# Performance work log

Hardware: AMD Instinct MI355X
Metric: run time of the kernel (lower is better)

The kernel has to match this reference:

```python
import jax, jax.numpy as jnp
import numpy as np
import math

IN_CH = 1024
OUT_CH = 512
T_DIM = 512
CLIP = 8
HEADS = 8
BS = 8192


def setup_inputs() -> dict:
    key = jax.random.key(0)
    ks = jax.random.split(key, 12)
    s = 0.02
    return {
        "x": jax.random.normal(ks[0], (BS * CLIP, IN_CH), dtype=jnp.float32),
        "t": jax.random.normal(ks[1], (BS, 1, T_DIM), dtype=jnp.float32),
        "W_down": jax.random.normal(ks[2], (OUT_CH, IN_CH), dtype=jnp.float32) * s,
        "b_down": jax.random.normal(ks[3], (OUT_CH,), dtype=jnp.float32) * s,
        "W_t": jax.random.normal(ks[4], (OUT_CH, T_DIM), dtype=jnp.float32) * s,
        "b_t": jax.random.normal(ks[5], (OUT_CH,), dtype=jnp.float32) * s,
        "W_qkv": jax.random.normal(ks[6], (3 * OUT_CH, OUT_CH), dtype=jnp.float32) * s,
        "b_qkv": jax.random.normal(ks[7], (3 * OUT_CH,), dtype=jnp.float32) * s,
        "W_out": jax.random.normal(ks[8], (OUT_CH, OUT_CH), dtype=jnp.float32) * s,
        "b_out": jax.random.normal(ks[9], (OUT_CH,), dtype=jnp.float32) * s,
    }


def reference(x, t, W_down, b_down, W_t, b_t, W_qkv, b_qkv, W_out, b_out):
    # down projection (in_channel != out_channels branch)
    x = x @ W_down.T + b_down                       # [bs*clip, out_ch]
    x = x.reshape(-1, CLIP, OUT_CH)                 # [bs, clip, out_ch]
    # time embedding (broadcast over clip dim)
    x = x + (t @ W_t.T + b_t)                       # [bs, clip, out_ch]
    qkv = x @ W_qkv.T + b_qkv                       # [bs, clip, 3*out_ch]
    bs, length, width = qkv.shape
    ch = width // (3 * HEADS)                       # 64
    q, k, v = jnp.split(qkv, 3, axis=2)             # each [bs, clip, out_ch]
    scale = 1.0 / math.sqrt(math.sqrt(ch))
    # NOTE: faithful to torch .view semantics (head-interleaved reshape)
    qh = (q * scale).reshape(bs * HEADS, length, ch)
    kh = (k * scale).reshape(bs * HEADS, length, ch)
    vh = v.reshape(bs * HEADS, length, ch)
    w = jnp.einsum('bqc,bkc->bqk', qh, kh)          # [bs*heads, clip, clip]
    w = jax.nn.softmax(w.astype(jnp.float32), axis=-1).astype(qkv.dtype)
    attn = jnp.einsum('bqk,bkc->bqc', w, vh).reshape(bs, length, -1)
    return attn @ W_out.T + b_out                   # [bs, clip, out_ch]
```

## Files before the change

### kernel.cpp

```cpp
#include <hip/hip_runtime.h>
#include <hip/hip_bf16.h>
#include <cstdint>
#include <cstddef>

typedef __bf16 bf16_t;
typedef __bf16 bf16x8 __attribute__((ext_vector_type(8)));
typedef float  f32x4  __attribute__((ext_vector_type(4)));

#define N_ROWS 65536
#define IN_CH  1024
#define OUT_CH 512
#define T_DIM  512
#define BS_    8192

__device__ __forceinline__ void async_copy16(const bf16_t* g, bf16_t* l) {
    __builtin_amdgcn_global_load_lds(
        (const __attribute__((address_space(1))) void*)(uintptr_t)(g),
        (__attribute__((address_space(3))) void*)(uintptr_t)(l),
        16, 0, 0);
}

__global__ __launch_bounds__(256)
void cvt_f32_bf16(const float* __restrict__ in, bf16_t* __restrict__ out, long n8) {
    long idx = (long)blockIdx.x * 256 + threadIdx.x;
    if (idx >= n8) return;
    const float4* p = (const float4*)(in + idx * 8);
    float4 u = p[0], v = p[1];
    bf16x8 o;
    o[0] = (__bf16)u.x; o[1] = (__bf16)u.y; o[2] = (__bf16)u.z; o[3] = (__bf16)u.w;
    o[4] = (__bf16)v.x; o[5] = (__bf16)v.y; o[6] = (__bf16)v.z; o[7] = (__bf16)v.w;
    *(bf16x8*)(out + idx * 8) = o;
}

__global__ __launch_bounds__(256)
void cvt_multi(const float* __restrict__ s0, bf16_t* __restrict__ d0, long n0,
               const float* __restrict__ s1, bf16_t* __restrict__ d1, long n1,
               const float* __restrict__ s2, bf16_t* __restrict__ d2, long n2,
               const float* __restrict__ s3, bf16_t* __restrict__ d3, long n3)
{
    long idx = (long)blockIdx.x * 256 + threadIdx.x;
    const float* s; bf16_t* d;
    if (idx < n0)                { s = s0; d = d0; }
    else if ((idx -= n0) < n1)   { s = s1; d = d1; }
    else if ((idx -= n1) < n2)   { s = s2; d = d2; }
    else if ((idx -= n2) < n3)   { s = s3; d = d3; }
    else return;
    const float4* p = (const float4*)(s + idx * 8);
    float4 u = p[0], v = p[1];
    bf16x8 o;
    o[0] = (__bf16)u.x; o[1] = (__bf16)u.y; o[2] = (__bf16)u.z; o[3] = (__bf16)u.w;
    o[4] = (__bf16)v.x; o[5] = (__bf16)v.y; o[6] = (__bf16)v.z; o[7] = (__bf16)v.w;
    *(bf16x8*)(d + idx * 8) = o;
}

__global__ __launch_bounds__(256)
void transpose_cvt(const float* __restrict__ in, bf16_t* __restrict__ out) {
    __shared__ float tile[64][65];
    const int bx = blockIdx.x;
    const int by = blockIdx.y;
    const int tx = threadIdx.x & 63;
    const int ty = threadIdx.x >> 6;
    #pragma unroll
    for (int r = 0; r < 64; r += 4)
        tile[r + ty][tx] = in[(size_t)(by * 64 + r + ty) * 1024 + bx * 64 + tx];
    __syncthreads();
    #pragma unroll
    for (int r = 0; r < 64; r += 4)
        out[(size_t)(bx * 64 + r + ty) * 512 + by * 64 + tx] = (bf16_t)tile[tx][r + ty];
}

template<int BIAS_MODE, typename CT>
__global__ __launch_bounds__(256, 3)
void gemm_bt(const bf16_t* __restrict__ A, const bf16_t* __restrict__ B,
             CT* __restrict__ C,
             const float* __restrict__ bias,
             const float* __restrict__ bias2,
             int M, int N, int K)
{
    __shared__ bf16_t sA[128 * 32];
    __shared__ bf16_t sB[128 * 32];

    const int tid  = threadIdx.x;
    const int wave = tid >> 6;
    const int lane = tid & 63;

    const int row0 = blockIdx.y * 128;
    const int col0 = blockIdx.x * 128;

    const int wr = (wave >> 1) * 64;
    const int wc = (wave & 1) * 64;

    f32x4 acc[4][4];
    #pragma unroll
    for (int i = 0; i < 4; ++i)
        #pragma unroll
        for (int j = 0; j < 4; ++j)
            acc[i][j] = (f32x4){0.f, 0.f, 0.f, 0.f};

    const int seg0  = wave * 2;
    const int srow  = lane >> 2;
    const int schnk = (lane & 3) * 8;

    const bf16_t* Abase = A + (size_t)row0 * K + (size_t)srow * K + schnk;
    const bf16_t* Bbase = B + (size_t)col0 * K + (size_t)srow * K + schnk;

    const int fr = lane & 15;
    const int fk = (lane >> 4) * 8;

    for (int k0 = 0; k0 < K; k0 += 32) {
        #pragma unroll
        for (int j2 = 0; j2 < 2; ++j2) {
            const int seg = seg0 + j2;
            async_copy16(Abase + (size_t)(seg * 16) * K + k0, sA + seg * 512);
            async_copy16(Bbase + (size_t)(seg * 16) * K + k0, sB + seg * 512);
        }
        __syncthreads();

        bf16x8 af[4], bfr[4];
        #pragma unroll
        for (int i = 0; i < 4; ++i)
            af[i] = *(const bf16x8*)(sA + (wr + i * 16 + fr) * 32 + fk);
        #pragma unroll
        for (int j = 0; j < 4; ++j)
            bfr[j] = *(const bf16x8*)(sB + (wc + j * 16 + fr) * 32 + fk);

        #pragma unroll
        for (int i = 0; i < 4; ++i)
            #pragma unroll
            for (int j = 0; j < 4; ++j)
                acc[i][j] = __builtin_amdgcn_mfma_f32_16x16x32_bf16(af[i], bfr[j], acc[i][j], 0, 0, 0);
        __syncthreads();
    }

    #pragma unroll
    for (int j = 0; j < 4; ++j) {
        const int gc = col0 + wc + j * 16 + (lane & 15);
        float cb = 0.f;
        if constexpr (BIAS_MODE == 0) cb = bias[gc];
        if constexpr (BIAS_MODE == 2) cb = bias[gc] + bias2[gc];
        #pragma unroll
        for (int i = 0; i < 4; ++i) {
            const int gr0 = row0 + wr + i * 16 + ((lane >> 4) << 2);
            #pragma unroll
            for (int r = 0; r < 4; ++r) {
                const int gr = gr0 + r;
                float v = acc[i][j][r];
                if constexpr (BIAS_MODE == 1)
                    v += bias2[(size_t)(gr >> 3) * N + gc];
                else
                    v += cb;
                C[(size_t)gr * N + gc] = (CT)v;
            }
        }
    }
}

__global__ __launch_bounds__(256, 4)
void attn_kernel(const bf16_t* __restrict__ qkv, bf16_t* __restrict__ out)
{
    __shared__ bf16_t skv[4][1024];
    const int tid  = threadIdx.x;
    const int wave = tid >> 6;
    const int lane = tid & 63;
    const size_t row = (size_t)blockIdx.x * 4 + wave;

    const bf16_t* base = qkv + row * 1536;
    bf16x8 q8 = *(const bf16x8*)(base + lane * 8);
    bf16x8 k8 = *(const bf16x8*)(base + 512 + lane * 8);
    bf16x8 v8 = *(const bf16x8*)(base + 1024 + lane * 8);
    *(bf16x8*)&skv[wave][lane * 8]       = k8;
    *(bf16x8*)&skv[wave][512 + lane * 8] = v8;

    float q[8];
    #pragma unroll
    for (int e = 0; e < 8; ++e) q[e] = (float)q8[e];
    __syncthreads();

    const int s8 = (lane & 7) * 8;
    float S[8];
    #pragma unroll
    for (int j = 0; j < 8; ++j) {
        bf16x8 kj = *(const bf16x8*)&skv[wave][j * 64 + s8];
        float p = 0.f;
        #pragma unroll
        for (int e = 0; e < 8; ++e) p += q[e] * (float)kj[e];
        p += __shfl_xor(p, 1);
        p += __shfl_xor(p, 2);
        p += __shfl_xor(p, 4);
        S[j] = p * 0.125f;
    }
    float m = S[0];
    #pragma unroll
    for (int j = 1; j < 8; ++j) m = fmaxf(m, S[j]);
    float sum = 0.f;
    #pragma unroll
    for (int j = 0; j < 8; ++j) { S[j] = __expf(S[j] - m); sum += S[j]; }
    const float inv = 1.f / sum;

    float o[8] = {0.f, 0.f, 0.f, 0.f, 0.f, 0.f, 0.f, 0.f};
    #pragma unroll
    for (int j = 0; j < 8; ++j) {
        const float pj = S[j] * inv;
        bf16x8 vj = *(const bf16x8*)&skv[wave][512 + j * 64 + s8];
        #pragma unroll
        for (int e = 0; e < 8; ++e) o[e] += pj * (float)vj[e];
    }
    bf16x8 o8;
    #pragma unroll
    for (int e = 0; e < 8; ++e) o8[e] = (__bf16)o[e];
    *(bf16x8*)(out + row * 512 + lane * 8) = o8;
}

extern "C" void kernel_launch(void* const* d_in, const int* in_sizes, int n_in,
                              void* d_out, int out_size, void* d_ws, size_t ws_size,
                              hipStream_t stream)
{
    const float* x      = (const float*)d_in[0];
    const float* t      = (const float*)d_in[1];
    const float* W_down = (const float*)d_in[2];
    const float* b_down = (const float*)d_in[3];
    const float* W_t    = (const float*)d_in[4];
    const float* b_t    = (const float*)d_in[5];
    const float* W_qkv  = (const float*)d_in[6];
    const float* b_qkv  = (const float*)d_in[7];
    const float* W_out  = (const float*)d_in[8];
    const float* b_out  = (const float*)d_in[9];
    float* out = (float*)d_out;

    char* p = (char*)d_ws;
    bf16_t* xb     = (bf16_t*)(p);
    bf16_t* qkvm   = (bf16_t*)(p + 134217728);
    bf16_t* am     = (bf16_t*)(p + 335544320);
    float*  tbias2 = (float*) (p + 402653184);
    bf16_t* tin    = (bf16_t*)(p + 452984832);
    bf16_t* tb     = (bf16_t*)(p + 461373440);
    bf16_t* wdT    = (bf16_t*)(p + 469762048);
    bf16_t* wt     = (bf16_t*)(p + 470810624);
    bf16_t* wq     = (bf16_t*)(p + 471334912);
    bf16_t* wo     = (bf16_t*)(p + 472907776);
    bf16_t* wf     = (bf16_t*)(p + 473432064);

    cvt_f32_bf16<<<32768, 256, 0, stream>>>(x, xb, (long)N_ROWS * IN_CH / 8);
    cvt_multi<<<2688, 256, 0, stream>>>(
        t,     tin, (long)BS_ * T_DIM / 8,
        W_qkv, wq,  (long)3 * OUT_CH * OUT_CH / 8,
        W_t,   wt,  (long)OUT_CH * T_DIM / 8,
        W_out, wo,  (long)OUT_CH * OUT_CH / 8);
    transpose_cvt<<<dim3(16, 8), 256, 0, stream>>>(W_down, wdT);

    gemm_bt<3, bf16_t><<<dim3(8, 12), 256, 0, stream>>>(
        wq, wdT, wf, nullptr, nullptr, 3 * OUT_CH, IN_CH, OUT_CH);

    gemm_bt<2, bf16_t><<<dim3(4, 64), 256, 0, stream>>>(
        tin, wt, tb, b_t, b_down, BS_, OUT_CH, T_DIM);

    gemm_bt<0, float><<<dim3(12, 64), 256, 0, stream>>>(
        tb, wq, tbias2, b_qkv, nullptr, BS_, 3 * OUT_CH, OUT_CH);

    gemm_bt<1, bf16_t><<<dim3(12, 512), 256, 0, stream>>>(
        xb, wf, qkvm, nullptr, tbias2, N_ROWS, 3 * OUT_CH, IN_CH);

    attn_kernel<<<16384, 256, 0, stream>>>(qkvm, am);

    gemm_bt<0, float><<<dim3(4, 512), 256, 0, stream>>>(
        am, wo, out, b_out, nullptr, N_ROWS, OUT_CH, OUT_CH);
}
```

Before: 873.4 us.

## Fuse attention with output projection and swizzle GEMM LDS tiles

Attention now writes its per-row outputs into shared memory, and the same block then runs the output-projection GEMM on those 32 rows with the full 512-wide W_out. This removes the round trip of the intermediate attention tensor through global memory and one kernel launch. The generic GEMM also gets an XOR swizzle on its LDS tiles to cut bank conflicts, and the broadcast time-bias in mode 1 is staged once in shared memory instead of being read from global memory per element. In exchange, the fused kernel uses more LDS, runs at lower occupancy, and does the attention part serially per wave with no overlap with the MFMA phase.

Result: slower. 894.4 us (+2.4%).

```diff
diff --git a/kernel.cpp b/kernel.cpp
--- a/kernel.cpp
+++ b/kernel.cpp
@@ -77,8 +77,9 @@
              const float* __restrict__ bias2,
              int M, int N, int K)
 {
-    __shared__ bf16_t sA[128 * 32];
-    __shared__ bf16_t sB[128 * 32];
+    __shared__ __align__(16) bf16_t sA[128 * 32];
+    __shared__ __align__(16) bf16_t sB[128 * 32];
+    __shared__ float stb[(BIAS_MODE == 1) ? 16 * 132 : 4];
 
     const int tid  = threadIdx.x;
     const int wave = tid >> 6;
@@ -90,6 +91,14 @@
     const int wr = (wave >> 1) * 64;
     const int wc = (wave & 1) * 64;
 
+    if constexpr (BIAS_MODE == 1) {
+        const int br = tid >> 4;
+        const int bc = (tid & 15) * 8;
+        const float* bsrc = bias2 + ((size_t)(row0 >> 3) + br) * N + col0 + bc;
+        *(float4*)&stb[br * 132 + bc]     = *(const float4*)(bsrc);
+        *(float4*)&stb[br * 132 + bc + 4] = *(const float4*)(bsrc + 4);
+    }
+
     f32x4 acc[4][4];
     #pragma unroll
     for (int i = 0; i < 4; ++i)
@@ -99,13 +108,14 @@
 
     const int seg0  = wave * 2;
     const int srow  = lane >> 2;
-    const int schnk = (lane & 3) * 8;
+    const int schnk = (((lane & 3) ^ (srow & 3)) * 8);
 
     const bf16_t* Abase = A + (size_t)row0 * K + (size_t)srow * K + schnk;
     const bf16_t* Bbase = B + (size_t)col0 * K + (size_t)srow * K + schnk;
 
     const int fr = lane & 15;
-    const int fk = (lane >> 4) * 8;
+    const int hi = lane >> 4;
+    const int swz = (hi ^ (fr & 3)) * 8;
 
     for (int k0 = 0; k0 < K; k0 += 32) {
         #pragma unroll
@@ -119,10 +129,10 @@
         bf16x8 af[4], bfr[4];
         #pragma unroll
         for (int i = 0; i < 4; ++i)
-            af[i] = *(const bf16x8*)(sA + (wr + i * 16 + fr) * 32 + fk);
+            af[i] = *(const bf16x8*)(sA + (wr + i * 16 + fr) * 32 + swz);
         #pragma unroll
         for (int j = 0; j < 4; ++j)
-            bfr[j] = *(const bf16x8*)(sB + (wc + j * 16 + fr) * 32 + fk);
+            bfr[j] = *(const bf16x8*)(sB + (wc + j * 16 + fr) * 32 + swz);
 
         #pragma unroll
         for (int i = 0; i < 4; ++i)
@@ -134,81 +144,141 @@
 
     #pragma unroll
     for (int j = 0; j < 4; ++j) {
-        const int gc = col0 + wc + j * 16 + (lane & 15);
+        const int gc = col0 + wc + j * 16 + fr;
         float cb = 0.f;
         if constexpr (BIAS_MODE == 0) cb = bias[gc];
         if constexpr (BIAS_MODE == 2) cb = bias[gc] + bias2[gc];
         #pragma unroll
         for (int i = 0; i < 4; ++i) {
-            const int gr0 = row0 + wr + i * 16 + ((lane >> 4) << 2);
+            const int lr0 = wr + i * 16 + hi * 4;
             #pragma unroll
             for (int r = 0; r < 4; ++r) {
-                const int gr = gr0 + r;
                 float v = acc[i][j][r];
                 if constexpr (BIAS_MODE == 1)
-                    v += bias2[(size_t)(gr >> 3) * N + gc];
+                    v += stb[((lr0 + r) >> 3) * 132 + wc + j * 16 + fr];
                 else
                     v += cb;
-                C[(size_t)gr * N + gc] = (CT)v;
+                C[(size_t)(row0 + lr0 + r) * N + gc] = (CT)v;
             }
         }
     }
 }
 
-__global__ __launch_bounds__(256, 4)
-void attn_kernel(const bf16_t* __restrict__ qkv, bf16_t* __restrict__ out)
+__global__ __launch_bounds__(256, 2)
+void attn_out(const bf16_t* __restrict__ qkv, const bf16_t* __restrict__ Wo,
+              const float* __restrict__ bias, float* __restrict__ C)
 {
-    __shared__ bf16_t skv[4][1024];
+    __shared__ __align__(16) bf16_t sa[32 * 512];
+    __shared__ __align__(16) bf16_t sB[512 * 32];
+
     const int tid  = threadIdx.x;
     const int wave = tid >> 6;
     const int lane = tid & 63;
-    const size_t row = (size_t)blockIdx.x * 4 + wave;
-
-    const bf16_t* base = qkv + row * 1536;
-    bf16x8 q8 = *(const bf16x8*)(base + lane * 8);
-    bf16x8 k8 = *(const bf16x8*)(base + 512 + lane * 8);
-    bf16x8 v8 = *(const bf16x8*)(base + 1024 + lane * 8);
-    *(bf16x8*)&skv[wave][lane * 8]       = k8;
-    *(bf16x8*)&skv[wave][512 + lane * 8] = v8;
-
-    float q[8];
-    #pragma unroll
-    for (int e = 0; e < 8; ++e) q[e] = (float)q8[e];
+    const int row0 = blockIdx.x * 32;
+
+    bf16_t* kv = sB + wave * 1024;
+    for (int rr = 0; rr < 8; ++rr) {
+        const int r = wave * 8 + rr;
+        const bf16_t* base = qkv + (size_t)(row0 + r) * 1536;
+        bf16x8 q8 = *(const bf16x8*)(base + lane * 8);
+        bf16x8 k8 = *(const bf16x8*)(base + 512 + lane * 8);
+        bf16x8 v8 = *(const bf16x8*)(base + 1024 + lane * 8);
+        *(bf16x8*)(kv + lane * 8)       = k8;
+        *(bf16x8*)(kv + 512 + lane * 8) = v8;
+
+        float q[8];
+        #pragma unroll
+        for (int e = 0; e < 8; ++e) q[e] = (float)q8[e];
+
+        const int s8 = (lane & 7) * 8;
+        float S[8];
+        #pragma unroll
+        for (int j = 0; j < 8; ++j) {
+            bf16x8 kj = *(const bf16x8*)(kv + j * 64 + s8);
+            float p = 0.f;
+            #pragma unroll
+            for (int e = 0; e < 8; ++e) p += q[e] * (float)kj[e];
+            p += __shfl_xor(p, 1);
+            p += __shfl_xor(p, 2);
+            p += __shfl_xor(p, 4);
+            S[j] = p * 0.125f;
+        }
+        float m = S[0];
+        #pragma unroll
+        for (int j = 1; j < 8; ++j) m = fmaxf(m, S[j]);
+        float sum = 0.f;
+        #pragma unroll
+        for (int j = 0; j < 8; ++j) { S[j] = __expf(S[j] - m); sum += S[j]; }
+        const float inv = 1.f / sum;
+
+        float o[8] = {0.f, 0.f, 0.f, 0.f, 0.f, 0.f, 0.f, 0.f};
+        #pragma unroll
+        for (int j = 0; j < 8; ++j) {
+            const float pj = S[j] * inv;
+            bf16x8 vj = *(const bf16x8*)(kv + 512 + j * 64 + s8);
+            #pragma unroll
+            for (int e = 0; e < 8; ++e) o[e] += pj * (float)vj[e];
+        }
+        bf16x8 o8;
+        #pragma unroll
+        for (int e = 0; e < 8; ++e) o8[e] = (__bf16)o[e];
+        *(bf16x8*)(sa + r * 512 + ((lane ^ (r & 7)) * 8)) = o8;
+    }
     __syncthreads();
 
-    const int s8 = (lane & 7) * 8;
-    float S[8];
+    const int wc = wave << 7;
+    const int fr = lane & 15;
+    const int hi = lane >> 4;
+    const int srow  = lane >> 2;
+    const int schnk = (((lane & 3) ^ (srow & 3)) * 8);
+    const int swzB  = (hi ^ (fr & 3)) * 8;
+    const int swzA  = fr & 7;
+
+    f32x4 acc[2][8];
+    #pragma unroll
+    for (int i = 0; i < 2; ++i)
+        #pragma unroll
+        for (int j = 0; j < 8; ++j)
+            acc[i][j] = (f32x4){0.f, 0.f, 0.f, 0.f};
+
+    for (int k0 = 0; k0 < 512; k0 += 32) {
+        #pragma unroll
+        for (int c = 0; c < 8; ++c) {
+            const int rowb = wc + c * 16;
+            async_copy16(Wo + (size_t)(rowb + srow) * 512 + k0 + schnk,
+                         sB + (size_t)rowb * 32);
+        }
+        __syncthreads();
+
+        bf16x8 af[2], bfr[8];
+        const int qc = (k0 >> 3) + hi;
+        #pragma unroll
+        for (int i = 0; i < 2; ++i)
+            af[i] = *(const bf16x8*)(sa + (i * 16 + fr) * 512 + ((qc ^ swzA) * 8));
+        #pragma unroll
+        for (int j = 0; j < 8; ++j)
+            bfr[j] = *(const bf16x8*)(sB + (wc + j * 16 + fr) * 32 + swzB);
+
+        #pragma unroll
+        for (int i = 0; i < 2; ++i)
+            #pragma unroll
+            for (int j = 0; j < 8; ++j)
+                acc[i][j] = __builtin_amdgcn_mfma_f32_16x16x32_bf16(af[i], bfr[j], acc[i][j], 0, 0, 0);
+        __syncthreads();
+    }
+
     #pragma unroll
     for (int j = 0; j < 8; ++j) {
-        bf16x8 kj = *(const bf16x8*)&skv[wave][j * 64 + s8];
-        float p = 0.f;
-        #pragma unroll
-        for (int e = 0; e < 8; ++e) p += q[e] * (float)kj[e];
-        p += __shfl_xor(p, 1);
-        p += __shfl_xor(p, 2);
-        p += __shfl_xor(p, 4);
-        S[j] = p * 0.125f;
-    }
-    float m = S[0];
-    #pragma unroll
-    for (int j = 1; j < 8; ++j) m = fmaxf(m, S[j]);
-    float sum = 0.f;
-    #pragma unroll
-    for (int j = 0; j < 8; ++j) { S[j] = __expf(S[j] - m); sum += S[j]; }
-    const float inv = 1.f / sum;
-
-    float o[8] = {0.f, 0.f, 0.f, 0.f, 0.f, 0.f, 0.f, 0.f};
-    #pragma unroll
-    for (int j = 0; j < 8; ++j) {
-        const float pj = S[j] * inv;
-        bf16x8 vj = *(const bf16x8*)&skv[wave][512 + j * 64 + s8];
-        #pragma unroll
-        for (int e = 0; e < 8; ++e) o[e] += pj * (float)vj[e];
-    }
-    bf16x8 o8;
-    #pragma unroll
-    for (int e = 0; e < 8; ++e) o8[e] = (__bf16)o[e];
-    *(bf16x8*)(out + row * 512 + lane * 8) = o8;
+        const int gc = wc + j * 16 + fr;
+        const float cb = bias[gc];
+        #pragma unroll
+        for (int i = 0; i < 2; ++i) {
+            const int gr0 = row0 + i * 16 + hi * 4;
+            #pragma unroll
+            for (int r = 0; r < 4; ++r)
+                C[(size_t)(gr0 + r) * 512 + gc] = acc[i][j][r] + cb;
+        }
+    }
 }
 
 extern "C" void kernel_launch(void* const* d_in, const int* in_sizes, int n_in,
@@ -230,15 +300,14 @@
     char* p = (char*)d_ws;
     bf16_t* xb     = (bf16_t*)(p);
     bf16_t* qkvm   = (bf16_t*)(p + 134217728);
-    bf16_t* am     = (bf16_t*)(p + 335544320);
-    float*  tbias2 = (float*) (p + 402653184);
-    bf16_t* tin    = (bf16_t*)(p + 452984832);
-    bf16_t* tb     = (bf16_t*)(p + 461373440);
-    bf16_t* wdT    = (bf16_t*)(p + 469762048);
-    bf16_t* wt     = (bf16_t*)(p + 470810624);
-    bf16_t* wq     = (bf16_t*)(p + 471334912);
-    bf16_t* wo     = (bf16_t*)(p + 472907776);
-    bf16_t* wf     = (bf16_t*)(p + 473432064);
+    float*  tbias2 = (float*) (p + 335544320);
+    bf16_t* tin    = (bf16_t*)(p + 385875968);
+    bf16_t* tb     = (bf16_t*)(p + 394264576);
+    bf16_t* wdT    = (bf16_t*)(p + 402653184);
+    bf16_t* wt     = (bf16_t*)(p + 403701760);
+    bf16_t* wq     = (bf16_t*)(p + 404226048);
+    bf16_t* wo     = (bf16_t*)(p + 405798912);
+    bf16_t* wf     = (bf16_t*)(p + 406323200);
 
     cvt_f32_bf16<<<32768, 256, 0, stream>>>(x, xb, (long)N_ROWS * IN_CH / 8);
     cvt_multi<<<2688, 256, 0, stream>>>(
@@ -260,8 +329,5 @@
     gemm_bt<1, bf16_t><<<dim3(12, 512), 256, 0, stream>>>(
         xb, wf, qkvm, nullptr, tbias2, N_ROWS, 3 * OUT_CH, IN_CH);
 
-    attn_kernel<<<16384, 256, 0, stream>>>(qkvm, am);
-
-    gemm_bt<0, float><<<dim3(4, 512), 256, 0, stream>>>(
-        am, wo, out, b_out, nullptr, N_ROWS, OUT_CH, OUT_CH);
-}
+    attn_out<<<2048, 256, 0, stream>>>(qkvm, wo, b_out, out);
+}
```
